# Performance work log

Measured on AMD Instinct MI355X. Metric: run time of the kernel, lower is better.

The kernel has to match this reference:

```python
import jax, jax.numpy as jnp
import numpy as np

B, S, D, H = 2, 2048, 1024, 16
DK = D // H  # 64


def setup_inputs() -> dict:
    key = jax.random.key(0)
    ks = jax.random.split(key, 11)
    scale = 1.0 / np.sqrt(D)
    inp = {
        "x": jax.random.normal(ks[0], (B, S, D), dtype=jnp.float32),
        "z": jax.random.normal(ks[1], (B, S, D), dtype=jnp.float32),
        # causal mask, broadcast over batch and heads; masked_fill where mask==0
        "mask": jnp.tril(jnp.ones((1, 1, S, S), dtype=jnp.int32)),
        "wq_w": jax.random.normal(ks[2], (D, D), dtype=jnp.float32) * scale,
        "wq_b": jax.random.normal(ks[3], (D,), dtype=jnp.float32) * 0.01,
        "wk_w": jax.random.normal(ks[4], (D, D), dtype=jnp.float32) * scale,
        "wk_b": jax.random.normal(ks[5], (D,), dtype=jnp.float32) * 0.01,
        "wv_w": jax.random.normal(ks[6], (D, D), dtype=jnp.float32) * scale,
        "wv_b": jax.random.normal(ks[7], (D,), dtype=jnp.float32) * 0.01,
        "wo_w": jax.random.normal(ks[8], (D, D), dtype=jnp.float32) * scale,
        "wo_b": jax.random.normal(ks[9], (D,), dtype=jnp.float32) * 0.01,
    }
    return inp


def reference(x, z, mask, wq_w, wq_b, wk_w, wk_b, wv_w, wv_b, wo_w, wo_b):
    # torch Linear: y = x @ W.T + b
    q = x @ wq_w.T + wq_b
    k = z @ wk_w.T + wk_b
    # NOTE: faithful to source bug: value uses wk, not wv (wv is a dead param)
    v = z @ wk_w.T + wk_b

    def split_heads(t):  # [B,S,D] -> [B,H,S,DK]
        return t.reshape(B, S, H, DK).transpose(0, 2, 1, 3)

    q, k, v = split_heads(q), split_heads(k), split_heads(v)

    scores = jnp.einsum("bhqd,bhkd->bhqk", q, k) * (DK ** -0.5)
    scores = jnp.where(mask == 0, -jnp.inf, scores)
    attn_weights = jax.nn.softmax(scores, axis=-1)  # [B,H,S,S]
    atn = jnp.einsum("bhqk,bhkd->bhqd", attn_weights, v)

    concat = atn.transpose(0, 2, 1, 3).reshape(B, S, D)
    output = concat @ wo_w.T + wo_b  # dropout rate 0.0 -> identity
    concat_attn_weight = attn_weights.sum(axis=1)  # [B,S,S]
    return output, concat_attn_weight
```

## Files before the change

kernel.cpp:

```cpp
#include <hip/hip_runtime.h>

typedef __bf16 bf16_t;
typedef __bf16 bf16x4 __attribute__((ext_vector_type(4)));
typedef __bf16 bf16x8 __attribute__((ext_vector_type(8)));
typedef float  f32x4  __attribute__((ext_vector_type(4)));

#define MFMA(a, b, c) __builtin_amdgcn_mfma_f32_16x16x32_bf16((a), (b), (c), 0, 0, 0)

static constexpr int Bsz = 2, S = 2048, D = 1024, H = 16, DK = 64;

__device__ __forceinline__ bf16x8 ld8(const bf16_t* p) { return *(const bf16x8*)p; }
__device__ __forceinline__ bf16x8 ld8(const float* p) {
    float4 a = *(const float4*)p;
    float4 b = *(const float4*)(p + 4);
    bf16x8 r;
    r[0] = (bf16_t)a.x; r[1] = (bf16_t)a.y; r[2] = (bf16_t)a.z; r[3] = (bf16_t)a.w;
    r[4] = (bf16_t)b.x; r[5] = (bf16_t)b.y; r[6] = (bf16_t)b.z; r[7] = (bf16_t)b.w;
    return r;
}

template <typename TA, typename TB, typename TC, int WRITE_KT>
__global__ __launch_bounds__(256) void gemm_bt(
    const TA* __restrict__ A, const TB* __restrict__ B,
    const float* __restrict__ bias, TC* __restrict__ C,
    bf16_t* __restrict__ KTout, int M, int N, int K)
{
    __shared__ bf16_t As[128][40];
    __shared__ bf16_t Bs[128][40];

    const int t    = threadIdx.x;
    const int wave = t >> 6, lane = t & 63;
    const int quad = lane >> 4, l15 = lane & 15;
    const int wm = (wave >> 1) * 64, wn = (wave & 1) * 64;
    const int rowbase = blockIdx.y * 128, colbase = blockIdx.x * 128;

    f32x4 acc[4][4];
#pragma unroll
    for (int i = 0; i < 4; ++i)
#pragma unroll
        for (int j = 0; j < 4; ++j) acc[i][j] = {0.f, 0.f, 0.f, 0.f};

    for (int kt = 0; kt < K; kt += 32) {
        __syncthreads();
#pragma unroll
        for (int c = 0; c < 2; ++c) {
            int f  = t + 256 * c;
            int r  = f >> 2;
            int cc = (f & 3) << 3;
            *(bf16x8*)&As[r][cc] = ld8(&A[(size_t)(rowbase + r) * K + kt + cc]);
            *(bf16x8*)&Bs[r][cc] = ld8(&B[(size_t)(colbase + r) * K + kt + cc]);
        }
        __syncthreads();

        bf16x8 af[4], bfr[4];
#pragma unroll
        for (int mt = 0; mt < 4; ++mt)
            af[mt] = *(const bf16x8*)&As[wm + mt * 16 + l15][quad * 8];
#pragma unroll
        for (int nt = 0; nt < 4; ++nt)
            bfr[nt] = *(const bf16x8*)&Bs[wn + nt * 16 + l15][quad * 8];
#pragma unroll
        for (int mt = 0; mt < 4; ++mt)
#pragma unroll
            for (int nt = 0; nt < 4; ++nt)
                acc[mt][nt] = MFMA(af[mt], bfr[nt], acc[mt][nt]);
    }

#pragma unroll
    for (int nt = 0; nt < 4; ++nt) {
        int col  = colbase + wn + nt * 16 + l15;
        float bv = bias[col];
#pragma unroll
        for (int mt = 0; mt < 4; ++mt) {
            int row0 = rowbase + wm + mt * 16 + quad * 4;
#pragma unroll
            for (int r = 0; r < 4; ++r) {
                float v = acc[mt][nt][r] + bv;
                C[(size_t)(row0 + r) * N + col] = (TC)v;
                if (WRITE_KT) {
                    int row = row0 + r;
                    int bb = row >> 11, srow = row & (S - 1);
                    int hh = col >> 6,  dd   = col & 63;
                    KTout[(((size_t)bb * H + hh) * DK + dd) * S + srow] = (bf16_t)v;
                }
            }
        }
    }
}

__global__ __launch_bounds__(256) void attn_flash(
    const bf16_t* __restrict__ Q, const bf16_t* __restrict__ Km,
    const bf16_t* __restrict__ KT,
    bf16_t* __restrict__ Oc, float* __restrict__ m_ws, float* __restrict__ il_ws)
{
    const int h = blockIdx.y, b = blockIdx.z;
    const int t = threadIdx.x;
    const int wave = t >> 6, lane = t & 63;
    const int quad = lane >> 4, l15 = lane & 15;

    __shared__ bf16_t Ks[2][64][72];
    __shared__ bf16_t KTs[2][64][72];
    __shared__ bf16_t PQ[64][72];

    const int hcol = h * DK;
    const bf16_t* KTh = KT + ((size_t)(b * H + h)) * DK * S;
    const size_t bS = (size_t)b * S;

    const int jr = (t >> 3);
    const int ce = (t & 7) * 8;

    for (int half = 0; half < 2; ++half) {
        const int qt = half == 0 ? (int)blockIdx.x : 31 - (int)blockIdx.x;
        const size_t qrow0 = bS + (size_t)qt * 64;

        __syncthreads();
        bf16x8 qld[2], kreg[2], ktreg[2];
#pragma unroll
        for (int p = 0; p < 2; ++p) {
            qld[p]   = *(const bf16x8*)&Q[(qrow0 + p * 32 + jr) * D + hcol + ce];
            kreg[p]  = *(const bf16x8*)&Km[(bS + p * 32 + jr) * D + hcol + ce];
            ktreg[p] = *(const bf16x8*)&KTh[(size_t)(p * 32 + jr) * S + ce];
        }
#pragma unroll
        for (int p = 0; p < 2; ++p) {
            *(bf16x8*)&PQ[p * 32 + jr][ce]       = qld[p];
            *(bf16x8*)&Ks[0][p * 32 + jr][ce]    = kreg[p];
            *(bf16x8*)&KTs[0][p * 32 + jr][ce]   = ktreg[p];
        }
        __syncthreads();
        const bf16x8 qf0 = *(const bf16x8*)&PQ[wave * 16 + l15][quad * 8];
        const bf16x8 qf1 = *(const bf16x8*)&PQ[wave * 16 + l15][32 + quad * 8];

        f32x4 accO[4];
#pragma unroll
        for (int u = 0; u < 4; ++u) accO[u] = {0.f, 0.f, 0.f, 0.f};
        float m_cur = -1e30f, l_cur = 0.f;

        const int iloc = wave * 16 + l15;

        for (int jt = 0; jt <= qt; ++jt) {
            const int cur = jt & 1, nxt = cur ^ 1;

            if (jt < qt) {
#pragma unroll
                for (int p = 0; p < 2; ++p) {
                    kreg[p]  = *(const bf16x8*)&Km[(bS + (size_t)(jt + 1) * 64 + p * 32 + jr) * D + hcol + ce];
                    ktreg[p] = *(const bf16x8*)&KTh[(size_t)(p * 32 + jr) * S + (size_t)(jt + 1) * 64 + ce];
                }
            }

            f32x4 sv[4];
#pragma unroll
            for (int nt = 0; nt < 4; ++nt) {
                bf16x8 a0 = *(const bf16x8*)&Ks[cur][nt * 16 + l15][quad * 8];
                bf16x8 a1 = *(const bf16x8*)&Ks[cur][nt * 16 + l15][32 + quad * 8];
                f32x4 a = {0.f, 0.f, 0.f, 0.f};
                a = MFMA(a0, qf0, a);
                a = MFMA(a1, qf1, a);
                sv[nt] = a;
            }

            const bool diag = (jt == qt);
#pragma unroll
            for (int nt = 0; nt < 4; ++nt)
#pragma unroll
                for (int r = 0; r < 4; ++r) {
                    float s = sv[nt][r] * 0.125f;
                    if (diag && (nt * 16 + quad * 4 + r) > iloc) s = -1e30f;
                    sv[nt][r] = s;
                }

            float tm = sv[0][0];
#pragma unroll
            for (int nt = 0; nt < 4; ++nt)
#pragma unroll
                for (int r = 0; r < 4; ++r) tm = fmaxf(tm, sv[nt][r]);
            tm = fmaxf(tm, __shfl_xor(tm, 16));
            tm = fmaxf(tm, __shfl_xor(tm, 32));
            float m_new = fmaxf(m_cur, tm);
            float alpha = __expf(m_cur - m_new);
            m_cur = m_new;
            float rs = 0.f;
#pragma unroll
            for (int nt = 0; nt < 4; ++nt)
#pragma unroll
                for (int r = 0; r < 4; ++r) {
                    float p = __expf(sv[nt][r] - m_new);
                    sv[nt][r] = p;
                    rs += p;
                }
            rs += __shfl_xor(rs, 16);
            rs += __shfl_xor(rs, 32);
            l_cur = l_cur * alpha + rs;

            float alpha4[4];
#pragma unroll
            for (int r = 0; r < 4; ++r)
                alpha4[r] = __shfl(alpha, (quad << 4) + quad * 4 + r, 64);
#pragma unroll
            for (int u = 0; u < 4; ++u)
#pragma unroll
                for (int r = 0; r < 4; ++r) accO[u][r] *= alpha4[r];

#pragma unroll
            for (int nt = 0; nt < 4; ++nt) {
                bf16x4 pk;
                pk[0] = (bf16_t)sv[nt][0]; pk[1] = (bf16_t)sv[nt][1];
                pk[2] = (bf16_t)sv[nt][2]; pk[3] = (bf16_t)sv[nt][3];
                *(bf16x4*)&PQ[wave * 16 + l15][nt * 16 + quad * 4] = pk;
            }
            asm volatile("s_waitcnt lgkmcnt(0)" ::: "memory");

            bf16x8 pa0 = *(const bf16x8*)&PQ[wave * 16 + l15][quad * 8];
            bf16x8 pa1 = *(const bf16x8*)&PQ[wave * 16 + l15][32 + quad * 8];
#pragma unroll
            for (int u = 0; u < 4; ++u) {
                bf16x8 v0 = *(const bf16x8*)&KTs[cur][u * 16 + l15][quad * 8];
                bf16x8 v1 = *(const bf16x8*)&KTs[cur][u * 16 + l15][32 + quad * 8];
                accO[u] = MFMA(pa0, v0, accO[u]);
                accO[u] = MFMA(pa1, v1, accO[u]);
            }

            if (jt < qt) {
#pragma unroll
                for (int p = 0; p < 2; ++p) {
                    *(bf16x8*)&Ks[nxt][p * 32 + jr][ce]  = kreg[p];
                    *(bf16x8*)&KTs[nxt][p * 32 + jr][ce] = ktreg[p];
                }
            }
            __syncthreads();
        }

        float invl = 1.f / l_cur;
        float invl4[4];
#pragma unroll
        for (int r = 0; r < 4; ++r)
            invl4[r] = __shfl(invl, (quad << 4) + quad * 4 + r, 64);
#pragma unroll
        for (int u = 0; u < 4; ++u)
#pragma unroll
            for (int r = 0; r < 4; ++r)
                Oc[(qrow0 + wave * 16 + quad * 4 + r) * D + hcol + u * 16 + l15] =
                    (bf16_t)(accO[u][r] * invl4[r]);

        if (quad == 0) {
            size_t sb = ((size_t)(b * H + h)) * S + (size_t)qt * 64 + wave * 16 + l15;
            m_ws[sb]  = m_cur;
            il_ws[sb] = invl;
        }
    }
}

__global__ __launch_bounds__(256) void attn_wsum(
    const bf16_t* __restrict__ Q, const bf16_t* __restrict__ Km,
    const float* __restrict__ m_ws, const float* __restrict__ il_ws,
    float* __restrict__ out2)
{
    const int jt = blockIdx.x, qt = blockIdx.y, b = blockIdx.z;
    const int t  = threadIdx.x;
    float* tile = out2 + (size_t)b * S * S + (size_t)qt * 64 * S + (size_t)jt * 64;

    if (jt > qt) {
        int r0 = t >> 2, c0 = (t & 3) * 16;
#pragma unroll
        for (int e = 0; e < 16; ++e) tile[(size_t)r0 * S + c0 + e] = 0.f;
        return;
    }

    const int wave = t >> 6, lane = t & 63;
    const int quad = lane >> 4, l15 = lane & 15;
    __shared__ bf16_t Ks[2][64][72];
    __shared__ bf16_t Qs[2][64][72];

    const int jr = (t >> 3), ce = (t & 7) * 8;
    const size_t krow = (size_t)b * S + (size_t)jt * 64;
    const size_t qrow = (size_t)b * S + (size_t)qt * 64;

    f32x4 accs[4];
#pragma unroll
    for (int nt = 0; nt < 4; ++nt) accs[nt] = {0.f, 0.f, 0.f, 0.f};

    bf16x8 kreg[2], qreg[2];
#pragma unroll
    for (int p = 0; p < 2; ++p) {
        kreg[p] = *(const bf16x8*)&Km[(krow + p * 32 + jr) * D + ce];
        qreg[p] = *(const bf16x8*)&Q[(qrow + p * 32 + jr) * D + ce];
    }
#pragma unroll
    for (int p = 0; p < 2; ++p) {
        *(bf16x8*)&Ks[0][p * 32 + jr][ce] = kreg[p];
        *(bf16x8*)&Qs[0][p * 32 + jr][ce] = qreg[p];
    }
    __syncthreads();

    for (int h = 0; h < H; ++h) {
        const int cur = h & 1, nxt = cur ^ 1;

        if (h < H - 1) {
            const int hc = (h + 1) * DK;
#pragma unroll
            for (int p = 0; p < 2; ++p) {
                kreg[p] = *(const bf16x8*)&Km[(krow + p * 32 + jr) * D + hc + ce];
                qreg[p] = *(const bf16x8*)&Q[(qrow + p * 32 + jr) * D + hc + ce];
            }
        }

        bf16x8 qf0 = *(const bf16x8*)&Qs[cur][wave * 16 + l15][quad * 8];
        bf16x8 qf1 = *(const bf16x8*)&Qs[cur][wave * 16 + l15][32 + quad * 8];

        size_t mlb = ((size_t)(b * H + h)) * S + (size_t)qt * 64 + wave * 16 + quad * 4;
        f32x4 mr = *(const f32x4*)&m_ws[mlb];
        f32x4 il = *(const f32x4*)&il_ws[mlb];

#pragma unroll
        for (int nt = 0; nt < 4; ++nt) {
            bf16x8 k0 = *(const bf16x8*)&Ks[cur][nt * 16 + l15][quad * 8];
            bf16x8 k1 = *(const bf16x8*)&Ks[cur][nt * 16 + l15][32 + quad * 8];
            f32x4 a = {0.f, 0.f, 0.f, 0.f};
            a = MFMA(qf0, k0, a);
            a = MFMA(qf1, k1, a);
#pragma unroll
            for (int r = 0; r < 4; ++r) {
                int i = qt * 64 + wave * 16 + quad * 4 + r;
                int j = jt * 64 + nt * 16 + l15;
                float p = (j <= i) ? __expf(a[r] * 0.125f - mr[r]) * il[r] : 0.f;
                accs[nt][r] += p;
            }
        }

        if (h < H - 1) {
#pragma unroll
            for (int p = 0; p < 2; ++p) {
                *(bf16x8*)&Ks[nxt][p * 32 + jr][ce] = kreg[p];
                *(bf16x8*)&Qs[nxt][p * 32 + jr][ce] = qreg[p];
            }
        }
        __syncthreads();
    }

#pragma unroll
    for (int nt = 0; nt < 4; ++nt)
#pragma unroll
        for (int r = 0; r < 4; ++r)
            tile[(size_t)(wave * 16 + quad * 4 + r) * S + nt * 16 + l15] = accs[nt][r];
}

extern "C" void kernel_launch(void* const* d_in, const int* in_sizes, int n_in,
                              void* d_out, int out_size, void* d_ws, size_t ws_size,
                              hipStream_t stream)
{
    const float* x    = (const float*)d_in[0];
    const float* z    = (const float*)d_in[1];
    const float* wq_w = (const float*)d_in[3];
    const float* wq_b = (const float*)d_in[4];
    const float* wk_w = (const float*)d_in[5];
    const float* wk_b = (const float*)d_in[6];
    const float* wo_w = (const float*)d_in[9];
    const float* wo_b = (const float*)d_in[10];

    float* out  = (float*)d_out;
    float* out2 = out + (size_t)Bsz * S * D;

    float*  m_ws  = (float*)d_ws;
    float*  il_ws = m_ws + (size_t)Bsz * H * S;
    bf16_t* Qws   = (bf16_t*)(il_ws + (size_t)Bsz * H * S);
    bf16_t* Kws   = Qws + (size_t)Bsz * S * D;
    bf16_t* Cc    = (bf16_t*)out2;
    bf16_t* KTws  = Cc + (size_t)Bsz * S * D;

    dim3 blk(256);
    gemm_bt<float, float, bf16_t, 0>
        <<<dim3(D / 128, (Bsz * S) / 128, 1), blk, 0, stream>>>(
            x, wq_w, wq_b, Qws, nullptr, Bsz * S, D, D);
    gemm_bt<float, float, bf16_t, 1>
        <<<dim3(D / 128, (Bsz * S) / 128, 1), blk, 0, stream>>>(
            z, wk_w, wk_b, Kws, KTws, Bsz * S, D, D);
    attn_flash<<<dim3(S / 128, H, Bsz), blk, 0, stream>>>(
        Qws, Kws, KTws, Cc, m_ws, il_ws);
    gemm_bt<bf16_t, float, float, 0>
        <<<dim3(D / 128, (Bsz * S) / 128, 1), blk, 0, stream>>>(
            Cc, wo_w, wo_b, out, nullptr, Bsz * S, D, D);
    attn_wsum<<<dim3(S / 64, S / 64, Bsz), blk, 0, stream>>>(
        Qws, Kws, m_ws, il_ws, out2);
}
```

Baseline: 325.9 us.

## Double-buffer GEMM tiles, merge Q/K projections, fold softmax scale into Q

The Q and K projection GEMMs now run as a single launch, with blockIdx.z choosing the operands. The GEMMs move to 512-thread blocks with double-buffered LDS: the next K-slice is loaded into registers while the current one feeds the MFMAs, so each iteration needs one barrier instead of two. The 1/sqrt(dk) scale is folded into the Q projection epilogue, which removes the per-score multiply in both attention kernels. The causal diagonal tile is peeled out of the flash loop so the off-diagonal iterations carry no mask check. In exchange, each thread holds fewer accumulators but more staging registers and LDS.

```diff
diff --git a/kernel.cpp b/kernel.cpp
--- a/kernel.cpp
+++ b/kernel.cpp
@@ -9,61 +9,81 @@
 
 static constexpr int Bsz = 2, S = 2048, D = 1024, H = 16, DK = 64;
 
-__device__ __forceinline__ bf16x8 ld8(const bf16_t* p) { return *(const bf16x8*)p; }
-__device__ __forceinline__ bf16x8 ld8(const float* p) {
-    float4 a = *(const float4*)p;
-    float4 b = *(const float4*)(p + 4);
+__device__ __forceinline__ bf16x8 pack8(float4 a, float4 b) {
     bf16x8 r;
     r[0] = (bf16_t)a.x; r[1] = (bf16_t)a.y; r[2] = (bf16_t)a.z; r[3] = (bf16_t)a.w;
     r[4] = (bf16_t)b.x; r[5] = (bf16_t)b.y; r[6] = (bf16_t)b.z; r[7] = (bf16_t)b.w;
     return r;
 }
 
-template <typename TA, typename TB, typename TC, int WRITE_KT>
-__global__ __launch_bounds__(256) void gemm_bt(
-    const TA* __restrict__ A, const TB* __restrict__ B,
-    const float* __restrict__ bias, TC* __restrict__ C,
-    bf16_t* __restrict__ KTout, int M, int N, int K)
+__global__ __launch_bounds__(512) void gemm_qk(
+    const float* __restrict__ xA, const float* __restrict__ wqB,
+    const float* __restrict__ wqb, bf16_t* __restrict__ Qc,
+    const float* __restrict__ zA, const float* __restrict__ wkB,
+    const float* __restrict__ wkb, bf16_t* __restrict__ Kc,
+    bf16_t* __restrict__ KTout)
 {
-    __shared__ bf16_t As[128][40];
-    __shared__ bf16_t Bs[128][40];
+    constexpr int M = Bsz * S, N = D, K = D;
+    const int zi = blockIdx.z;
+    const float* A    = zi ? zA  : xA;
+    const float* B    = zi ? wkB : wqB;
+    const float* bias = zi ? wkb : wqb;
+    bf16_t*      C    = zi ? Kc  : Qc;
+    const float  sc   = zi ? 1.f : 0.125f;
+
+    __shared__ bf16_t As[2][128][40];
+    __shared__ bf16_t Bs[2][128][40];
 
     const int t    = threadIdx.x;
     const int wave = t >> 6, lane = t & 63;
     const int quad = lane >> 4, l15 = lane & 15;
-    const int wm = (wave >> 1) * 64, wn = (wave & 1) * 64;
+    const int wm = (wave >> 1) * 32, wn = (wave & 1) * 64;
     const int rowbase = blockIdx.y * 128, colbase = blockIdx.x * 128;
-
-    f32x4 acc[4][4];
-#pragma unroll
-    for (int i = 0; i < 4; ++i)
+    const int r  = t >> 2;
+    const int cc = (t & 3) << 3;
+
+    f32x4 acc[2][4];
+#pragma unroll
+    for (int i = 0; i < 2; ++i)
 #pragma unroll
         for (int j = 0; j < 4; ++j) acc[i][j] = {0.f, 0.f, 0.f, 0.f};
 
+    float4 a0 = *(const float4*)&A[(size_t)(rowbase + r) * K + cc];
+    float4 a1 = *(const float4*)&A[(size_t)(rowbase + r) * K + cc + 4];
+    float4 b0 = *(const float4*)&B[(size_t)(colbase + r) * K + cc];
+    float4 b1 = *(const float4*)&B[(size_t)(colbase + r) * K + cc + 4];
+    *(bf16x8*)&As[0][r][cc] = pack8(a0, a1);
+    *(bf16x8*)&Bs[0][r][cc] = pack8(b0, b1);
+    __syncthreads();
+
     for (int kt = 0; kt < K; kt += 32) {
-        __syncthreads();
-#pragma unroll
-        for (int c = 0; c < 2; ++c) {
-            int f  = t + 256 * c;
-            int r  = f >> 2;
-            int cc = (f & 3) << 3;
-            *(bf16x8*)&As[r][cc] = ld8(&A[(size_t)(rowbase + r) * K + kt + cc]);
-            *(bf16x8*)&Bs[r][cc] = ld8(&B[(size_t)(colbase + r) * K + kt + cc]);
-        }
-        __syncthreads();
-
-        bf16x8 af[4], bfr[4];
-#pragma unroll
-        for (int mt = 0; mt < 4; ++mt)
-            af[mt] = *(const bf16x8*)&As[wm + mt * 16 + l15][quad * 8];
+        const int cur = (kt >> 5) & 1, nxt = cur ^ 1;
+        const bool more = (kt + 32) < K;
+        if (more) {
+            a0 = *(const float4*)&A[(size_t)(rowbase + r) * K + kt + 32 + cc];
+            a1 = *(const float4*)&A[(size_t)(rowbase + r) * K + kt + 32 + cc + 4];
+            b0 = *(const float4*)&B[(size_t)(colbase + r) * K + kt + 32 + cc];
+            b1 = *(const float4*)&B[(size_t)(colbase + r) * K + kt + 32 + cc + 4];
+        }
+
+        bf16x8 af[2], bfr[4];
+#pragma unroll
+        for (int mt = 0; mt < 2; ++mt)
+            af[mt] = *(const bf16x8*)&As[cur][wm + mt * 16 + l15][quad * 8];
 #pragma unroll
         for (int nt = 0; nt < 4; ++nt)
-            bfr[nt] = *(const bf16x8*)&Bs[wn + nt * 16 + l15][quad * 8];
-#pragma unroll
-        for (int mt = 0; mt < 4; ++mt)
+            bfr[nt] = *(const bf16x8*)&Bs[cur][wn + nt * 16 + l15][quad * 8];
+#pragma unroll
+        for (int mt = 0; mt < 2; ++mt)
 #pragma unroll
             for (int nt = 0; nt < 4; ++nt)
                 acc[mt][nt] = MFMA(af[mt], bfr[nt], acc[mt][nt]);
+
+        if (more) {
+            *(bf16x8*)&As[nxt][r][cc] = pack8(a0, a1);
+            *(bf16x8*)&Bs[nxt][r][cc] = pack8(b0, b1);
+        }
+        __syncthreads();
     }
 
 #pragma unroll
@@ -71,19 +91,91 @@
         int col  = colbase + wn + nt * 16 + l15;
         float bv = bias[col];
 #pragma unroll
-        for (int mt = 0; mt < 4; ++mt) {
+        for (int mt = 0; mt < 2; ++mt) {
             int row0 = rowbase + wm + mt * 16 + quad * 4;
 #pragma unroll
-            for (int r = 0; r < 4; ++r) {
-                float v = acc[mt][nt][r] + bv;
-                C[(size_t)(row0 + r) * N + col] = (TC)v;
-                if (WRITE_KT) {
-                    int row = row0 + r;
+            for (int rr = 0; rr < 4; ++rr) {
+                float v = (acc[mt][nt][rr] + bv) * sc;
+                C[(size_t)(row0 + rr) * N + col] = (bf16_t)v;
+                if (zi) {
+                    int row = row0 + rr;
                     int bb = row >> 11, srow = row & (S - 1);
                     int hh = col >> 6,  dd   = col & 63;
                     KTout[(((size_t)bb * H + hh) * DK + dd) * S + srow] = (bf16_t)v;
                 }
             }
+        }
+    }
+}
+
+__global__ __launch_bounds__(512) void gemm_obt(
+    const bf16_t* __restrict__ A, const float* __restrict__ B,
+    const float* __restrict__ bias, float* __restrict__ C)
+{
+    constexpr int M = Bsz * S, N = D, K = D;
+    __shared__ bf16_t As[2][128][40];
+    __shared__ bf16_t Bs[2][128][40];
+
+    const int t    = threadIdx.x;
+    const int wave = t >> 6, lane = t & 63;
+    const int quad = lane >> 4, l15 = lane & 15;
+    const int wm = (wave >> 1) * 32, wn = (wave & 1) * 64;
+    const int rowbase = blockIdx.y * 128, colbase = blockIdx.x * 128;
+    const int r  = t >> 2;
+    const int cc = (t & 3) << 3;
+
+    f32x4 acc[2][4];
+#pragma unroll
+    for (int i = 0; i < 2; ++i)
+#pragma unroll
+        for (int j = 0; j < 4; ++j) acc[i][j] = {0.f, 0.f, 0.f, 0.f};
+
+    bf16x8 areg = *(const bf16x8*)&A[(size_t)(rowbase + r) * K + cc];
+    float4 b0   = *(const float4*)&B[(size_t)(colbase + r) * K + cc];
+    float4 b1   = *(const float4*)&B[(size_t)(colbase + r) * K + cc + 4];
+    *(bf16x8*)&As[0][r][cc] = areg;
+    *(bf16x8*)&Bs[0][r][cc] = pack8(b0, b1);
+    __syncthreads();
+
+    for (int kt = 0; kt < K; kt += 32) {
+        const int cur = (kt >> 5) & 1, nxt = cur ^ 1;
+        const bool more = (kt + 32) < K;
+        if (more) {
+            areg = *(const bf16x8*)&A[(size_t)(rowbase + r) * K + kt + 32 + cc];
+            b0   = *(const float4*)&B[(size_t)(colbase + r) * K + kt + 32 + cc];
+            b1   = *(const float4*)&B[(size_t)(colbase + r) * K + kt + 32 + cc + 4];
+        }
+
+        bf16x8 af[2], bfr[4];
+#pragma unroll
+        for (int mt = 0; mt < 2; ++mt)
+            af[mt] = *(const bf16x8*)&As[cur][wm + mt * 16 + l15][quad * 8];
+#pragma unroll
+        for (int nt = 0; nt < 4; ++nt)
+            bfr[nt] = *(const bf16x8*)&Bs[cur][wn + nt * 16 + l15][quad * 8];
+#pragma unroll
+        for (int mt = 0; mt < 2; ++mt)
+#pragma unroll
+            for (int nt = 0; nt < 4; ++nt)
+                acc[mt][nt] = MFMA(af[mt], bfr[nt], acc[mt][nt]);
+
+        if (more) {
+            *(bf16x8*)&As[nxt][r][cc] = areg;
+            *(bf16x8*)&Bs[nxt][r][cc] = pack8(b0, b1);
+        }
+        __syncthreads();
+    }
+
+#pragma unroll
+    for (int nt = 0; nt < 4; ++nt) {
+        int col  = colbase + wn + nt * 16 + l15;
+        float bv = bias[col];
+#pragma unroll
+        for (int mt = 0; mt < 2; ++mt) {
+            int row0 = rowbase + wm + mt * 16 + quad * 4;
+#pragma unroll
+            for (int rr = 0; rr < 4; ++rr)
+                C[(size_t)(row0 + rr) * N + col] = acc[mt][nt][rr] + bv;
         }
     }
 }
@@ -108,6 +200,7 @@
 
     const int jr = (t >> 3);
     const int ce = (t & 7) * 8;
+    const int iloc = wave * 16 + l15;
 
     for (int half = 0; half < 2; ++half) {
         const int qt = half == 0 ? (int)blockIdx.x : 31 - (int)blockIdx.x;
@@ -123,9 +216,9 @@
         }
 #pragma unroll
         for (int p = 0; p < 2; ++p) {
-            *(bf16x8*)&PQ[p * 32 + jr][ce]       = qld[p];
-            *(bf16x8*)&Ks[0][p * 32 + jr][ce]    = kreg[p];
-            *(bf16x8*)&KTs[0][p * 32 + jr][ce]   = ktreg[p];
+            *(bf16x8*)&PQ[p * 32 + jr][ce]     = qld[p];
+            *(bf16x8*)&Ks[0][p * 32 + jr][ce]  = kreg[p];
+            *(bf16x8*)&KTs[0][p * 32 + jr][ce] = ktreg[p];
         }
         __syncthreads();
         const bf16x8 qf0 = *(const bf16x8*)&PQ[wave * 16 + l15][quad * 8];
@@ -136,40 +229,7 @@
         for (int u = 0; u < 4; ++u) accO[u] = {0.f, 0.f, 0.f, 0.f};
         float m_cur = -1e30f, l_cur = 0.f;
 
-        const int iloc = wave * 16 + l15;
-
-        for (int jt = 0; jt <= qt; ++jt) {
-            const int cur = jt & 1, nxt = cur ^ 1;
-
-            if (jt < qt) {
-#pragma unroll
-                for (int p = 0; p < 2; ++p) {
-                    kreg[p]  = *(const bf16x8*)&Km[(bS + (size_t)(jt + 1) * 64 + p * 32 + jr) * D + hcol + ce];
-                    ktreg[p] = *(const bf16x8*)&KTh[(size_t)(p * 32 + jr) * S + (size_t)(jt + 1) * 64 + ce];
-                }
-            }
-
-            f32x4 sv[4];
-#pragma unroll
-            for (int nt = 0; nt < 4; ++nt) {
-                bf16x8 a0 = *(const bf16x8*)&Ks[cur][nt * 16 + l15][quad * 8];
-                bf16x8 a1 = *(const bf16x8*)&Ks[cur][nt * 16 + l15][32 + quad * 8];
-                f32x4 a = {0.f, 0.f, 0.f, 0.f};
-                a = MFMA(a0, qf0, a);
-                a = MFMA(a1, qf1, a);
-                sv[nt] = a;
-            }
-
-            const bool diag = (jt == qt);
-#pragma unroll
-            for (int nt = 0; nt < 4; ++nt)
-#pragma unroll
-                for (int r = 0; r < 4; ++r) {
-                    float s = sv[nt][r] * 0.125f;
-                    if (diag && (nt * 16 + quad * 4 + r) > iloc) s = -1e30f;
-                    sv[nt][r] = s;
-                }
-
+        auto softmax_pv = [&](f32x4 sv[4], int cur) {
             float tm = sv[0][0];
 #pragma unroll
             for (int nt = 0; nt < 4; ++nt)
@@ -220,15 +280,52 @@
                 accO[u] = MFMA(pa0, v0, accO[u]);
                 accO[u] = MFMA(pa1, v1, accO[u]);
             }
-
-            if (jt < qt) {
-#pragma unroll
-                for (int p = 0; p < 2; ++p) {
-                    *(bf16x8*)&Ks[nxt][p * 32 + jr][ce]  = kreg[p];
-                    *(bf16x8*)&KTs[nxt][p * 32 + jr][ce] = ktreg[p];
-                }
+        };
+
+        for (int jt = 0; jt < qt; ++jt) {
+            const int cur = jt & 1, nxt = cur ^ 1;
+#pragma unroll
+            for (int p = 0; p < 2; ++p) {
+                kreg[p]  = *(const bf16x8*)&Km[(bS + (size_t)(jt + 1) * 64 + p * 32 + jr) * D + hcol + ce];
+                ktreg[p] = *(const bf16x8*)&KTh[(size_t)(p * 32 + jr) * S + (size_t)(jt + 1) * 64 + ce];
+            }
+
+            f32x4 sv[4];
+#pragma unroll
+            for (int nt = 0; nt < 4; ++nt) {
+                bf16x8 a0 = *(const bf16x8*)&Ks[cur][nt * 16 + l15][quad * 8];
+                bf16x8 a1 = *(const bf16x8*)&Ks[cur][nt * 16 + l15][32 + quad * 8];
+                f32x4 a = {0.f, 0.f, 0.f, 0.f};
+                a = MFMA(a0, qf0, a);
+                a = MFMA(a1, qf1, a);
+                sv[nt] = a;
+            }
+            softmax_pv(sv, cur);
+
+#pragma unroll
+            for (int p = 0; p < 2; ++p) {
+                *(bf16x8*)&Ks[nxt][p * 32 + jr][ce]  = kreg[p];
+                *(bf16x8*)&KTs[nxt][p * 32 + jr][ce] = ktreg[p];
             }
             __syncthreads();
+        }
+
+        {
+            const int cur = qt & 1;
+            f32x4 sv[4];
+#pragma unroll
+            for (int nt = 0; nt < 4; ++nt) {
+                bf16x8 a0 = *(const bf16x8*)&Ks[cur][nt * 16 + l15][quad * 8];
+                bf16x8 a1 = *(const bf16x8*)&Ks[cur][nt * 16 + l15][32 + quad * 8];
+                f32x4 a = {0.f, 0.f, 0.f, 0.f};
+                a = MFMA(a0, qf0, a);
+                a = MFMA(a1, qf1, a);
+#pragma unroll
+                for (int r = 0; r < 4; ++r)
+                    if ((nt * 16 + quad * 4 + r) > iloc) a[r] = -1e30f;
+                sv[nt] = a;
+            }
+            softmax_pv(sv, cur);
         }
 
         float invl = 1.f / l_cur;
@@ -323,7 +420,7 @@
             for (int r = 0; r < 4; ++r) {
                 int i = qt * 64 + wave * 16 + quad * 4 + r;
                 int j = jt * 64 + nt * 16 + l15;
-                float p = (j <= i) ? __expf(a[r] * 0.125f - mr[r]) * il[r] : 0.f;
+                float p = (j <= i) ? __expf(a[r] - mr[r]) * il[r] : 0.f;
                 accs[nt][r] += p;
             }
         }
@@ -368,18 +465,12 @@
     bf16_t* Cc    = (bf16_t*)out2;
     bf16_t* KTws  = Cc + (size_t)Bsz * S * D;
 
-    dim3 blk(256);
-    gemm_bt<float, float, bf16_t, 0>
-        <<<dim3(D / 128, (Bsz * S) / 128, 1), blk, 0, stream>>>(
-            x, wq_w, wq_b, Qws, nullptr, Bsz * S, D, D);
-    gemm_bt<float, float, bf16_t, 1>
-        <<<dim3(D / 128, (Bsz * S) / 128, 1), blk, 0, stream>>>(
-            z, wk_w, wk_b, Kws, KTws, Bsz * S, D, D);
-    attn_flash<<<dim3(S / 128, H, Bsz), blk, 0, stream>>>(
+    gemm_qk<<<dim3(D / 128, (Bsz * S) / 128, 2), dim3(512), 0, stream>>>(
+        x, wq_w, wq_b, Qws, z, wk_w, wk_b, Kws, KTws);
+    attn_flash<<<dim3(S / 128, H, Bsz), dim3(256), 0, stream>>>(
         Qws, Kws, KTws, Cc, m_ws, il_ws);
-    gemm_bt<bf16_t, float, float, 0>
-        <<<dim3(D / 128, (Bsz * S) / 128, 1), blk, 0, stream>>>(
-            Cc, wo_w, wo_b, out, nullptr, Bsz * S, D, D);
-    attn_wsum<<<dim3(S / 64, S / 64, Bsz), blk, 0, stream>>>(
+    gemm_obt<<<dim3(D / 128, (Bsz * S) / 128, 1), dim3(512), 0, stream>>>(
+        Cc, wo_w, wo_b, out);
+    attn_wsum<<<dim3(S / 64, S / 64, Bsz), dim3(256), 0, stream>>>(
         Qws, Kws, m_ws, il_ws, out2);
 }
```

New measurement: 286.8 us. 1.14x faster.
